# Kernel tuning notes

Hardware: AMD Instinct MI355X
Metric: run time of the kernel (lower is better)

Reference implementation:

```python
import jax, jax.numpy as jnp
import numpy as np

B, L = 128, 4096
H, RH, D, K = 128, 64, 64, 512  # num_hiddens, residual_hiddens, embedding_dim, num_embeddings
BETA = 0.25  # commitment_cost


def conv1d(x, w, b=None, stride=1, pad=0):
    # x: (N, C, W); w: (O, I, K) torch layout
    y = jax.lax.conv_general_dilated(x, w, (stride,), [(pad, pad)],
                                     dimension_numbers=('NCW', 'OIW', 'NCW'))
    return y if b is None else y + b[None, :, None]


def convT1d(x, w, b=None, stride=2, pad=1):
    # torch ConvTranspose1d weight layout (in, out, k)
    k = w.shape[-1]
    w_t = jnp.flip(w, -1).transpose(1, 0, 2)  # (out, in, k)
    y = jax.lax.conv_general_dilated(x, w_t, (1,), [(k - 1 - pad, k - 1 - pad)],
                                     lhs_dilation=(stride,),
                                     dimension_numbers=('NCW', 'OIW', 'NCW'))
    return y if b is None else y + b[None, :, None]


def res_stack(x, layers):
    for w1, w2 in layers:
        h = conv1d(jax.nn.relu(x), w1, None, 1, 1)
        h = conv1d(jax.nn.relu(h), w2, None, 1, 0)
        x = x + h
    return jax.nn.relu(x)


def _forward(x, enc_w1, enc_b1, enc_w2, enc_b2, enc_w3, enc_b3,
             enc_r1a, enc_r1b, enc_r2a, enc_r2b, pre_vq_w, pre_vq_b, codebook,
             dec_w1, dec_b1, dec_r1a, dec_r1b, dec_r2a, dec_r2b,
             dec_ct1_w, dec_ct1_b, dec_ct2_w, dec_ct2_b):
    # ---- Encoder (compression_factor == 4) ----
    h = x[:, None, :]                                   # (B, 1, L)
    h = jax.nn.relu(conv1d(h, enc_w1, enc_b1, 2, 1))    # (B, H/2, L/2)
    h = jax.nn.relu(conv1d(h, enc_w2, enc_b2, 2, 1))    # (B, H, L/4)
    h = conv1d(h, enc_w3, enc_b3, 1, 1)
    h = res_stack(h, [(enc_r1a, enc_r1b), (enc_r2a, enc_r2b)])
    z = conv1d(h, pre_vq_w, pre_vq_b, 1, 0)             # (B, D, T)

    # ---- Vector quantization ----
    zt = z.transpose(0, 2, 1)                           # (B, T, D)
    flat = zt.reshape(-1, D)                            # (BT, D)
    dists = (jnp.sum(flat * flat, 1, keepdims=True)
             - 2.0 * flat @ codebook.T
             + jnp.sum(codebook * codebook, 1))         # (BT, K)
    idx = jnp.argmin(dists, axis=1)                     # (BT,)
    q = codebook[idx].reshape(zt.shape)                 # (B, T, D)

    e_latent = jnp.mean((jax.lax.stop_gradient(q) - zt) ** 2)
    q_latent = jnp.mean((q - jax.lax.stop_gradient(zt)) ** 2)
    loss = q_latent + BETA * e_latent
    q_st = zt + jax.lax.stop_gradient(q - zt)           # straight-through

    counts = jnp.zeros((K,), flat.dtype).at[idx].add(1.0)
    probs = counts / idx.shape[0]
    perplexity = jnp.exp(-jnp.sum(probs * jnp.log(probs + 1e-10)))

    # ---- Decoder (compression_factor == 4) ----
    hd = q_st.transpose(0, 2, 1)                        # (B, D, T)
    hd = conv1d(hd, dec_w1, dec_b1, 1, 1)               # (B, H, T)
    hd = res_stack(hd, [(dec_r1a, dec_r1b), (dec_r2a, dec_r2b)])
    hd = jax.nn.relu(convT1d(hd, dec_ct1_w, dec_ct1_b)) # (B, H/2, 2T)
    hd = convT1d(hd, dec_ct2_w, dec_ct2_b)              # (B, 1, 4T)
    recon = jnp.squeeze(hd)                             # (B, L)
    return loss, recon, perplexity


def setup_inputs() -> dict:
    key = jax.random.key(0)
    ks = jax.random.split(key, 32)
    n = lambda i, shape, s=0.05: jax.random.normal(ks[i], shape, jnp.float32) * s
    inp = {
        'x': jax.random.normal(ks[0], (B, L), jnp.float32),
        'enc_w1': n(1, (H // 2, 1, 4)), 'enc_b1': jnp.zeros((H // 2,), jnp.float32),
        'enc_w2': n(2, (H, H // 2, 4)), 'enc_b2': jnp.zeros((H,), jnp.float32),
        'enc_w3': n(3, (H, H, 3)), 'enc_b3': jnp.zeros((H,), jnp.float32),
        'enc_r1a': n(4, (RH, H, 3)), 'enc_r1b': n(5, (H, RH, 1)),
        'enc_r2a': n(6, (RH, H, 3)), 'enc_r2b': n(7, (H, RH, 1)),
        'pre_vq_w': n(8, (D, H, 1)), 'pre_vq_b': jnp.zeros((D,), jnp.float32),
        'codebook': jax.random.uniform(ks[9], (K, D), jnp.float32, -1.0 / K, 1.0 / K),
        'dec_w1': n(10, (H, D, 3)), 'dec_b1': jnp.zeros((H,), jnp.float32),
        'dec_r1a': n(11, (RH, H, 3)), 'dec_r1b': n(12, (H, RH, 1)),
        'dec_r2a': n(13, (RH, H, 3)), 'dec_r2b': n(14, (H, RH, 1)),
        'dec_ct1_w': n(15, (H, H // 2, 4)), 'dec_ct1_b': jnp.zeros((H // 2,), jnp.float32),
        'dec_ct2_w': n(16, (H // 2, 1, 4)), 'dec_ct2_b': jnp.zeros((1,), jnp.float32),
    }
    return inp


def reference(x, enc_w1, enc_b1, enc_w2, enc_b2, enc_w3, enc_b3,
              enc_r1a, enc_r1b, enc_r2a, enc_r2b, pre_vq_w, pre_vq_b, codebook,
              dec_w1, dec_b1, dec_r1a, dec_r1b, dec_r2a, dec_r2b,
              dec_ct1_w, dec_ct1_b, dec_ct2_w, dec_ct2_b):
    return _forward(x, enc_w1, enc_b1, enc_w2, enc_b2, enc_w3, enc_b3,
                    enc_r1a, enc_r1b, enc_r2a, enc_r2b, pre_vq_w, pre_vq_b, codebook,
                    dec_w1, dec_b1, dec_r1a, dec_r1b, dec_r2a, dec_r2b,
                    dec_ct1_w, dec_ct1_b, dec_ct2_w, dec_ct2_b)
```

## Files before the change

kernel.cpp:

```cpp
#include <hip/hip_runtime.h>
#include <hip/hip_bf16.h>
#include <math.h>

using bf16 = __hip_bfloat16;
typedef __attribute__((ext_vector_type(4))) float f32x4;
typedef __attribute__((ext_vector_type(8))) short s16x8;

#define MFMA16(a,b,c) __builtin_amdgcn_mfma_f32_16x16x32_bf16((a),(b),(c),0,0,0)


__device__ inline float bf2f(unsigned short u) {
    union { float f; unsigned v; } c; c.v = ((unsigned)u) << 16; return c.f;
}
__device__ inline unsigned short bfbits(float f) {
    union { bf16 h; unsigned short u; } c; c.h = __float2bfloat16(f); return c.u;
}
__device__ inline s16x8 relu8(s16x8 v) {
#pragma unroll
    for (int j = 0; j < 8; ++j)
        v[j] = (short)(((unsigned short)v[j] & 0x8000u) ? 0 : (unsigned short)v[j]);
    return v;
}

__global__ __launch_bounds__(256, 3) void encmid_k(
    const bf16* __restrict__ in, const bf16* __restrict__ w3t,
    const float* __restrict__ b3, const bf16* __restrict__ r1w1,
    const bf16* __restrict__ r1w2, const bf16* __restrict__ r2w1,
    const bf16* __restrict__ r2w2, bf16* __restrict__ out)
{
    __shared__ __align__(16) char smem[47872];
    char* sY = smem;
    char* sX = smem + 21760;
    char* sH = smem + 21760;
    const int tid = threadIdx.x;
    const int b   = blockIdx.y;
    const int l0  = blockIdx.x * 64;
    const bf16* inb = in + (size_t)b * 1024 * 128;

    for (int i = tid; i < 96 * 16; i += 256) {
        int t = i >> 4, c0 = (i & 15) * 8;
        int g = l0 - 16 + t;
        s16x8 v = {};
        if (g >= 0 && g < 1024) v = *(const s16x8*)(inb + (size_t)g * 128 + c0);
        *(s16x8*)(sX + ((t * 136 + c0) << 1)) = v;
    }
    __syncthreads();

    const int lane = tid & 63;
    const int wid  = __builtin_amdgcn_readfirstlane(tid >> 6);
    const int lr   = lane & 15;
    const int kg   = lane >> 4;
    const f32x4 zf4 = {0.f, 0.f, 0.f, 0.f};

    {
        const int co0 = wid * 32;
        f32x4 acc[2][5];
#pragma unroll
        for (int cf = 0; cf < 2; ++cf)
#pragma unroll
            for (int lf = 0; lf < 5; ++lf) acc[cf][lf] = zf4;
#pragma unroll
        for (int k = 0; k < 3; ++k) {
            const bf16* Ab = w3t + (size_t)k * 128 * 128;
#pragma unroll
            for (int ks = 0; ks < 4; ++ks) {
                s16x8 af[2];
#pragma unroll
                for (int cf = 0; cf < 2; ++cf)
                    af[cf] = *(const s16x8*)(Ab + (co0 + cf * 16 + lr) * 128 + ks * 32 + kg * 8);
                s16x8 bfr[5];
#pragma unroll
                for (int lf = 0; lf < 5; ++lf) {
                    int tx = lf * 16 + lr + 7 + k;
                    bfr[lf] = *(const s16x8*)(sX + ((tx * 136 + ks * 32 + kg * 8) << 1));
                }
#pragma unroll
                for (int cf = 0; cf < 2; ++cf)
#pragma unroll
                    for (int lf = 0; lf < 5; ++lf)
                        acc[cf][lf] = MFMA16(af[cf], bfr[lf], acc[cf][lf]);
            }
        }
        __syncthreads();
#pragma unroll
        for (int cf = 0; cf < 2; ++cf)
#pragma unroll
            for (int lf = 0; lf < 5; ++lf) {
                int row = lf * 16 + lr;
                int p   = l0 - 8 + row;
                int cb0 = co0 + cf * 16 + kg * 4;
                bool ok = (p >= 0 && p < 1024);
                float r[4];
#pragma unroll
                for (int j = 0; j < 4; ++j)
                    r[j] = ok ? (acc[cf][lf][j] + b3[cb0 + j]) : 0.f;
                uint2 pk;
                pk.x = (unsigned)bfbits(r[0]) | ((unsigned)bfbits(r[1]) << 16);
                pk.y = (unsigned)bfbits(r[2]) | ((unsigned)bfbits(r[3]) << 16);
                *(uint2*)(sY + ((row * 136 + cb0) << 1)) = pk;
            }
    }
    __syncthreads();

#pragma unroll 1
    for (int blk = 0; blk < 2; ++blk) {
        const bf16* w1 = blk ? r2w1 : r1w1;
        {
            const int co0 = wid * 16;
            f32x4 acc[5];
#pragma unroll
            for (int lf = 0; lf < 5; ++lf) acc[lf] = zf4;
#pragma unroll
            for (int k = 0; k < 3; ++k) {
                const bf16* Ab = w1 + (size_t)k * 64 * 128;
#pragma unroll
                for (int ks = 0; ks < 4; ++ks) {
                    s16x8 a = *(const s16x8*)(Ab + (co0 + lr) * 128 + ks * 32 + kg * 8);
                    s16x8 bfr[5];
#pragma unroll
                    for (int lf = 0; lf < 5; ++lf) {
                        int ry = lf * 16 + lr + k - 1;
                        ry = (ry < 0) ? 0 : (ry > 79 ? 79 : ry);
                        bfr[lf] = relu8(*(const s16x8*)(sY + ((ry * 136 + ks * 32 + kg * 8) << 1)));
                    }
#pragma unroll
                    for (int lf = 0; lf < 5; ++lf)
                        acc[lf] = MFMA16(a, bfr[lf], acc[lf]);
                }
            }
#pragma unroll
            for (int lf = 0; lf < 5; ++lf) {
                int row = lf * 16 + lr;
                int ch0 = co0 + kg * 4;
                uint2 pk;
                pk.x = (unsigned)bfbits(fmaxf(acc[lf][0], 0.f)) |
                       ((unsigned)bfbits(fmaxf(acc[lf][1], 0.f)) << 16);
                pk.y = (unsigned)bfbits(fmaxf(acc[lf][2], 0.f)) |
                       ((unsigned)bfbits(fmaxf(acc[lf][3], 0.f)) << 16);
                *(uint2*)(sH + ((row * 72 + ch0) << 1)) = pk;
            }
        }
        __syncthreads();

        if (blk == 0) {
            const int co0 = wid * 32;
            f32x4 acc[2][5];
#pragma unroll
            for (int cf = 0; cf < 2; ++cf)
#pragma unroll
                for (int lf = 0; lf < 5; ++lf) acc[cf][lf] = zf4;
#pragma unroll
            for (int ks = 0; ks < 2; ++ks) {
                s16x8 af[2];
#pragma unroll
                for (int cf = 0; cf < 2; ++cf)
                    af[cf] = *(const s16x8*)(r1w2 + (size_t)(co0 + cf * 16 + lr) * 64 + ks * 32 + kg * 8);
                s16x8 bfr[5];
#pragma unroll
                for (int lf = 0; lf < 5; ++lf) {
                    int row = lf * 16 + lr;
                    bfr[lf] = *(const s16x8*)(sH + ((row * 72 + ks * 32 + kg * 8) << 1));
                }
#pragma unroll
                for (int cf = 0; cf < 2; ++cf)
#pragma unroll
                    for (int lf = 0; lf < 5; ++lf)
                        acc[cf][lf] = MFMA16(af[cf], bfr[lf], acc[cf][lf]);
            }
#pragma unroll
            for (int cf = 0; cf < 2; ++cf)
#pragma unroll
                for (int lf = 0; lf < 5; ++lf) {
                    int row = lf * 16 + lr;
                    int p   = l0 - 8 + row;
                    int cb0 = co0 + cf * 16 + kg * 4;
                    uint2 old = *(const uint2*)(sY + ((row * 136 + cb0) << 1));
                    bool ok = (p >= 0 && p < 1024);
                    float r[4];
                    r[0] = acc[cf][lf][0] + bf2f((unsigned short)(old.x & 0xffff));
                    r[1] = acc[cf][lf][1] + bf2f((unsigned short)(old.x >> 16));
                    r[2] = acc[cf][lf][2] + bf2f((unsigned short)(old.y & 0xffff));
                    r[3] = acc[cf][lf][3] + bf2f((unsigned short)(old.y >> 16));
                    uint2 pk;
                    pk.x = ok ? ((unsigned)bfbits(r[0]) | ((unsigned)bfbits(r[1]) << 16)) : 0u;
                    pk.y = ok ? ((unsigned)bfbits(r[2]) | ((unsigned)bfbits(r[3]) << 16)) : 0u;
                    *(uint2*)(sY + ((row * 136 + cb0) << 1)) = pk;
                }
            __syncthreads();
        } else {
            const int co0 = wid * 32;
            f32x4 acc[2][4];
#pragma unroll
            for (int cf = 0; cf < 2; ++cf)
#pragma unroll
                for (int lf = 0; lf < 4; ++lf) acc[cf][lf] = zf4;
#pragma unroll
            for (int ks = 0; ks < 2; ++ks) {
                s16x8 af[2];
#pragma unroll
                for (int cf = 0; cf < 2; ++cf)
                    af[cf] = *(const s16x8*)(r2w2 + (size_t)(co0 + cf * 16 + lr) * 64 + ks * 32 + kg * 8);
                s16x8 bfr[4];
#pragma unroll
                for (int lf = 0; lf < 4; ++lf) {
                    int row = 8 + lf * 16 + lr;
                    bfr[lf] = *(const s16x8*)(sH + ((row * 72 + ks * 32 + kg * 8) << 1));
                }
#pragma unroll
                for (int cf = 0; cf < 2; ++cf)
#pragma unroll
                    for (int lf = 0; lf < 4; ++lf)
                        acc[cf][lf] = MFMA16(af[cf], bfr[lf], acc[cf][lf]);
            }
#pragma unroll
            for (int cf = 0; cf < 2; ++cf)
#pragma unroll
                for (int lf = 0; lf < 4; ++lf) {
                    int row = 8 + lf * 16 + lr;
                    int cb0 = co0 + cf * 16 + kg * 4;
                    uint2 old = *(const uint2*)(sY + ((row * 136 + cb0) << 1));
                    float r[4];
                    r[0] = fmaxf(acc[cf][lf][0] + bf2f((unsigned short)(old.x & 0xffff)), 0.f);
                    r[1] = fmaxf(acc[cf][lf][1] + bf2f((unsigned short)(old.x >> 16)), 0.f);
                    r[2] = fmaxf(acc[cf][lf][2] + bf2f((unsigned short)(old.y & 0xffff)), 0.f);
                    r[3] = fmaxf(acc[cf][lf][3] + bf2f((unsigned short)(old.y >> 16)), 0.f);
                    uint2 pk;
                    pk.x = (unsigned)bfbits(r[0]) | ((unsigned)bfbits(r[1]) << 16);
                    pk.y = (unsigned)bfbits(r[2]) | ((unsigned)bfbits(r[3]) << 16);
                    *(uint2*)(out + ((size_t)b * 1024 + l0 + lf * 16 + lr) * 128 + cb0) = pk;
                }
        }
    }
}

__global__ __launch_bounds__(256, 4) void decmid_k(
    const bf16* __restrict__ qin, const bf16* __restrict__ dw1,
    const float* __restrict__ db1, const bf16* __restrict__ r1w1,
    const bf16* __restrict__ r1w2, const bf16* __restrict__ r2w1,
    const bf16* __restrict__ r2w2, const bf16* __restrict__ ct1w,
    const float* __restrict__ ct1b, bf16* __restrict__ out)
{
    __shared__ __align__(16) char smem[35584];
    char* sY = smem;
    char* sQ = smem + 21760;
    char* sH = smem + 21760;
    const int tid = threadIdx.x;
    const int b   = blockIdx.y;
    const int l0  = blockIdx.x * 64;
    const bf16* inb = qin + (size_t)b * 1024 * 64;

    for (int i = tid; i < 96 * 8; i += 256) {
        int t = i >> 3, c0 = (i & 7) * 8;
        int g = l0 - 16 + t;
        s16x8 v = {};
        if (g >= 0 && g < 1024) v = *(const s16x8*)(inb + (size_t)g * 64 + c0);
        *(s16x8*)(sQ + ((t * 72 + c0) << 1)) = v;
    }
    __syncthreads();

    const int lane = tid & 63;
    const int wid  = __builtin_amdgcn_readfirstlane(tid >> 6);
    const int lr   = lane & 15;
    const int kg   = lane >> 4;
    const f32x4 zf4 = {0.f, 0.f, 0.f, 0.f};

    {
        const int co0 = wid * 32;
        f32x4 acc[2][5];
#pragma unroll
        for (int cf = 0; cf < 2; ++cf)
#pragma unroll
            for (int lf = 0; lf < 5; ++lf) acc[cf][lf] = zf4;
#pragma unroll
        for (int k = 0; k < 3; ++k) {
            const bf16* Ab = dw1 + (size_t)k * 128 * 64;
#pragma unroll
            for (int ks = 0; ks < 2; ++ks) {
                s16x8 af[2];
#pragma unroll
                for (int cf = 0; cf < 2; ++cf)
                    af[cf] = *(const s16x8*)(Ab + (co0 + cf * 16 + lr) * 64 + ks * 32 + kg * 8);
                s16x8 bfr[5];
#pragma unroll
                for (int lf = 0; lf < 5; ++lf) {
                    int tx = lf * 16 + lr + 7 + k;
                    bfr[lf] = *(const s16x8*)(sQ + ((tx * 72 + ks * 32 + kg * 8) << 1));
                }
#pragma unroll
                for (int cf = 0; cf < 2; ++cf)
#pragma unroll
                    for (int lf = 0; lf < 5; ++lf)
                        acc[cf][lf] = MFMA16(af[cf], bfr[lf], acc[cf][lf]);
            }
        }
        __syncthreads();
#pragma unroll
        for (int cf = 0; cf < 2; ++cf)
#pragma unroll
            for (int lf = 0; lf < 5; ++lf) {
                int row = lf * 16 + lr;
                int p   = l0 - 8 + row;
                int cb0 = co0 + cf * 16 + kg * 4;
                bool ok = (p >= 0 && p < 1024);
                float r[4];
#pragma unroll
                for (int j = 0; j < 4; ++j)
                    r[j] = ok ? (acc[cf][lf][j] + db1[cb0 + j]) : 0.f;
                uint2 pk;
                pk.x = (unsigned)bfbits(r[0]) | ((unsigned)bfbits(r[1]) << 16);
                pk.y = (unsigned)bfbits(r[2]) | ((unsigned)bfbits(r[3]) << 16);
                *(uint2*)(sY + ((row * 136 + cb0) << 1)) = pk;
            }
    }
    __syncthreads();

#pragma unroll 1
    for (int blk = 0; blk < 2; ++blk) {
        const bf16* w1 = blk ? r2w1 : r1w1;
        const bf16* w2 = blk ? r2w2 : r1w2;
        {
            const int co0 = wid * 16;
            f32x4 acc[5];
#pragma unroll
            for (int lf = 0; lf < 5; ++lf) acc[lf] = zf4;
#pragma unroll
            for (int k = 0; k < 3; ++k) {
                const bf16* Ab = w1 + (size_t)k * 64 * 128;
#pragma unroll
                for (int ks = 0; ks < 4; ++ks) {
                    s16x8 a = *(const s16x8*)(Ab + (co0 + lr) * 128 + ks * 32 + kg * 8);
                    s16x8 bfr[5];
#pragma unroll
                    for (int lf = 0; lf < 5; ++lf) {
                        int ry = lf * 16 + lr + k - 1;
                        ry = (ry < 0) ? 0 : (ry > 79 ? 79 : ry);
                        bfr[lf] = relu8(*(const s16x8*)(sY + ((ry * 136 + ks * 32 + kg * 8) << 1)));
                    }
#pragma unroll
                    for (int lf = 0; lf < 5; ++lf)
                        acc[lf] = MFMA16(a, bfr[lf], acc[lf]);
                }
            }
#pragma unroll
            for (int lf = 0; lf < 5; ++lf) {
                int row = lf * 16 + lr;
                int ch0 = co0 + kg * 4;
                uint2 pk;
                pk.x = (unsigned)bfbits(fmaxf(acc[lf][0], 0.f)) |
                       ((unsigned)bfbits(fmaxf(acc[lf][1], 0.f)) << 16);
                pk.y = (unsigned)bfbits(fmaxf(acc[lf][2], 0.f)) |
                       ((unsigned)bfbits(fmaxf(acc[lf][3], 0.f)) << 16);
                *(uint2*)(sH + ((row * 72 + ch0) << 1)) = pk;
            }
        }
        __syncthreads();
        {
            const int co0 = wid * 32;
            f32x4 acc[2][5];
#pragma unroll
            for (int cf = 0; cf < 2; ++cf)
#pragma unroll
                for (int lf = 0; lf < 5; ++lf) acc[cf][lf] = zf4;
#pragma unroll
            for (int ks = 0; ks < 2; ++ks) {
                s16x8 af[2];
#pragma unroll
                for (int cf = 0; cf < 2; ++cf)
                    af[cf] = *(const s16x8*)(w2 + (size_t)(co0 + cf * 16 + lr) * 64 + ks * 32 + kg * 8);
                s16x8 bfr[5];
#pragma unroll
                for (int lf = 0; lf < 5; ++lf) {
                    int row = lf * 16 + lr;
                    bfr[lf] = *(const s16x8*)(sH + ((row * 72 + ks * 32 + kg * 8) << 1));
                }
#pragma unroll
                for (int cf = 0; cf < 2; ++cf)
#pragma unroll
                    for (int lf = 0; lf < 5; ++lf)
                        acc[cf][lf] = MFMA16(af[cf], bfr[lf], acc[cf][lf]);
            }
#pragma unroll
            for (int cf = 0; cf < 2; ++cf)
#pragma unroll
                for (int lf = 0; lf < 5; ++lf) {
                    int row = lf * 16 + lr;
                    int p   = l0 - 8 + row;
                    int cb0 = co0 + cf * 16 + kg * 4;
                    uint2 old = *(const uint2*)(sY + ((row * 136 + cb0) << 1));
                    bool ok = (p >= 0 && p < 1024);
                    float r[4];
                    r[0] = acc[cf][lf][0] + bf2f((unsigned short)(old.x & 0xffff));
                    r[1] = acc[cf][lf][1] + bf2f((unsigned short)(old.x >> 16));
                    r[2] = acc[cf][lf][2] + bf2f((unsigned short)(old.y & 0xffff));
                    r[3] = acc[cf][lf][3] + bf2f((unsigned short)(old.y >> 16));
                    if (blk == 1)
#pragma unroll
                        for (int j = 0; j < 4; ++j) r[j] = fmaxf(r[j], 0.f);
                    uint2 pk;
                    pk.x = ok ? ((unsigned)bfbits(r[0]) | ((unsigned)bfbits(r[1]) << 16)) : 0u;
                    pk.y = ok ? ((unsigned)bfbits(r[2]) | ((unsigned)bfbits(r[3]) << 16)) : 0u;
                    *(uint2*)(sY + ((row * 136 + cb0) << 1)) = pk;
                }
        }
        __syncthreads();
    }

    {
        const int co0 = (wid & 1) * 32;
        const int mh  = wid >> 1;
        f32x4 acc[2][2][2];
#pragma unroll
        for (int g = 0; g < 2; ++g)
#pragma unroll
            for (int cf = 0; cf < 2; ++cf)
#pragma unroll
                for (int j = 0; j < 2; ++j) acc[g][cf][j] = zf4;
#pragma unroll
        for (int g = 0; g < 2; ++g)
#pragma unroll
            for (int k = 0; k < 2; ++k) {
                const bf16* Ab = ct1w + (size_t)(g * 2 + k) * 64 * 128;
                const int doff = (g == 0) ? (k - 1) : k;
#pragma unroll
                for (int ks = 0; ks < 4; ++ks) {
                    s16x8 af[2];
#pragma unroll
                    for (int cf = 0; cf < 2; ++cf)
                        af[cf] = *(const s16x8*)(Ab + (co0 + cf * 16 + lr) * 128 + ks * 32 + kg * 8);
                    s16x8 bfr[2];
#pragma unroll
                    for (int j = 0; j < 2; ++j) {
                        int ty = 8 + (mh * 2 + j) * 16 + lr + doff;
                        bfr[j] = *(const s16x8*)(sY + ((ty * 136 + ks * 32 + kg * 8) << 1));
                    }
#pragma unroll
                    for (int cf = 0; cf < 2; ++cf)
#pragma unroll
                        for (int j = 0; j < 2; ++j)
                            acc[g][cf][j] = MFMA16(af[cf], bfr[j], acc[g][cf][j]);
                }
            }
#pragma unroll
        for (int g = 0; g < 2; ++g)
#pragma unroll
            for (int cf = 0; cf < 2; ++cf)
#pragma unroll
                for (int j = 0; j < 2; ++j) {
                    int m   = (mh * 2 + j) * 16 + lr;
                    int cb0 = co0 + cf * 16 + kg * 4;
                    float r[4];
#pragma unroll
                    for (int jj = 0; jj < 4; ++jj)
                        r[jj] = fmaxf(acc[g][cf][j][jj] + ct1b[cb0 + jj], 0.f);
                    uint2 pk;
                    pk.x = (unsigned)bfbits(r[0]) | ((unsigned)bfbits(r[1]) << 16);
                    pk.y = (unsigned)bfbits(r[2]) | ((unsigned)bfbits(r[3]) << 16);
                    *(uint2*)(out + ((size_t)b * 2048 + 2 * (l0 + m) + g) * 64 + cb0) = pk;
                }
    }
}

__global__ __launch_bounds__(256) void enc12_k(
    const float* __restrict__ x, const float* __restrict__ w1,
    const float* __restrict__ b1, const bf16* __restrict__ w2t,
    const float* __restrict__ b2, bf16* __restrict__ out)
{
    __shared__ float sXf[268];
    __shared__ float sW1[256];
    __shared__ float sB1[64];
    __shared__ __align__(16) char sX[132 * 144];
    const int tid = threadIdx.x;
    const int b   = blockIdx.y;
    const int l0  = blockIdx.x * 64;
    const float* xb = x + (size_t)b * 4096;

    for (int i = tid; i < 266; i += 256) {
        int g = 4 * l0 - 3 + i;
        sXf[i] = (g >= 0 && g < 4096) ? xb[g] : 0.f;
    }
    if (tid < 256) sW1[tid] = w1[tid];
    if (tid < 64)  sB1[tid] = b1[tid];
    __syncthreads();

    for (int i = tid; i < 132 * 64; i += 256) {
        int t = i >> 6, c = i & 63;
        int p = (t < 66) ? 2 * (l0 + t) : 2 * (l0 + t - 66) - 1;
        float v = 0.f;
        if (p >= 0 && p < 2048) {
            int xi = 2 * p - 4 * l0 + 2;
            float a = sB1[c];
#pragma unroll
            for (int k = 0; k < 4; ++k) a = fmaf(sXf[xi + k], sW1[c * 4 + k], a);
            v = fmaxf(a, 0.f);
        }
        *(bf16*)(sX + ((t * 72 + c) << 1)) = __float2bfloat16(v);
    }
    __syncthreads();

    const int lane = tid & 63;
    const int wid  = __builtin_amdgcn_readfirstlane(tid >> 6);
    const int co0  = wid * 32;
    const int lr   = lane & 15;
    const int kg   = lane >> 4;

    f32x4 acc[2][4];
#pragma unroll
    for (int cf = 0; cf < 2; ++cf)
#pragma unroll
        for (int lf = 0; lf < 4; ++lf) acc[cf][lf] = (f32x4){0.f, 0.f, 0.f, 0.f};

#pragma unroll
    for (int k = 0; k < 4; ++k) {
        const int roff = (k == 0) ? 66 : (k == 1) ? 0 : (k == 2) ? 67 : 1;
        const bf16* Ab = w2t + (size_t)k * 128 * 64;
#pragma unroll
        for (int ks = 0; ks < 2; ++ks) {
            s16x8 af[2];
#pragma unroll
            for (int cf = 0; cf < 2; ++cf)
                af[cf] = *(const s16x8*)(Ab + (co0 + cf * 16 + lr) * 64 + ks * 32 + kg * 8);
            s16x8 bfr[4];
#pragma unroll
            for (int lf = 0; lf < 4; ++lf) {
                int t = roff + lf * 16 + lr;
                bfr[lf] = *(const s16x8*)(sX + ((t * 72 + ks * 32 + kg * 8) << 1));
            }
#pragma unroll
            for (int cf = 0; cf < 2; ++cf)
#pragma unroll
                for (int lf = 0; lf < 4; ++lf)
                    acc[cf][lf] = MFMA16(af[cf], bfr[lf], acc[cf][lf]);
        }
    }

#pragma unroll
    for (int cf = 0; cf < 2; ++cf)
#pragma unroll
        for (int lf = 0; lf < 4; ++lf) {
            int cb0  = co0 + cf * 16 + kg * 4;
            int lcol = lf * 16 + lr;
            float r[4];
#pragma unroll
            for (int j = 0; j < 4; ++j)
                r[j] = fmaxf(acc[cf][lf][j] + b2[cb0 + j], 0.f);
            uint2 pk;
            pk.x = (unsigned)bfbits(r[0]) | ((unsigned)bfbits(r[1]) << 16);
            pk.y = (unsigned)bfbits(r[2]) | ((unsigned)bfbits(r[3]) << 16);
            *(uint2*)(out + ((size_t)b * 1024 + l0 + lcol) * 128 + cb0) = pk;
        }
}

__global__ __launch_bounds__(256) void ct2_k(
    const bf16* __restrict__ in, const float* __restrict__ w,
    const float* __restrict__ bias, float* __restrict__ out)
{
    __shared__ __align__(16) char sX[258 * 144];
    const int tid = threadIdx.x;
    const int b   = blockIdx.y;
    const int m0  = blockIdx.x * 256;
    const bf16* inb = in + (size_t)b * 2048 * 64;
    for (int i = tid; i < 258 * 8; i += 256) {
        int t = i >> 3, c0 = (i & 7) * 8;
        int g = m0 - 1 + t;
        s16x8 v = {};
        if (g >= 0 && g < 2048) v = *(const s16x8*)(inb + (size_t)g * 64 + c0);
        *(s16x8*)(sX + ((t * 72 + c0) << 1)) = v;
    }
    __syncthreads();
    float e = bias[0], o = bias[0];
#pragma unroll
    for (int c0 = 0; c0 < 64; c0 += 8) {
        s16x8 vm1 = *(const s16x8*)(sX + (((tid + 0) * 72 + c0) << 1));
        s16x8 v0  = *(const s16x8*)(sX + (((tid + 1) * 72 + c0) << 1));
        s16x8 vp1 = *(const s16x8*)(sX + (((tid + 2) * 72 + c0) << 1));
#pragma unroll
        for (int j = 0; j < 8; ++j) {
            int ci = c0 + j;
            float xm1 = bf2f((unsigned short)vm1[j]);
            float x0  = bf2f((unsigned short)v0[j]);
            float xp1 = bf2f((unsigned short)vp1[j]);
            e = fmaf(x0,  w[ci * 4 + 1], fmaf(xm1, w[ci * 4 + 3], e));
            o = fmaf(xp1, w[ci * 4 + 0], fmaf(x0,  w[ci * 4 + 2], o));
        }
    }
    int m = m0 + tid;
    out[(size_t)b * 4096 + 2 * m]     = e;
    out[(size_t)b * 4096 + 2 * m + 1] = o;
}

__global__ __launch_bounds__(256) void wx_k(
    const float* ew2, const float* ew3, const float* er1a, const float* er1b,
    const float* er2a, const float* er2b, const float* pvw, const float* dw1,
    const float* dr1a, const float* dr1b, const float* dr2a, const float* dr2b,
    const float* ct1w, bf16* wb)
{
    const int job = blockIdx.x;
    bf16* dst = wb + (size_t)job * 65536;
    const float* src; int CO, CI, K;
    switch (job) {
        case 0:  src = ew2;  CO = 128; CI = 64;  K = 4; break;
        case 1:  src = ew3;  CO = 128; CI = 128; K = 3; break;
        case 2:  src = er1a; CO = 64;  CI = 128; K = 3; break;
        case 3:  src = er1b; CO = 128; CI = 64;  K = 1; break;
        case 4:  src = er2a; CO = 64;  CI = 128; K = 3; break;
        case 5:  src = er2b; CO = 128; CI = 64;  K = 1; break;
        case 6:  src = pvw;  CO = 64;  CI = 128; K = 1; break;
        case 7:  src = dw1;  CO = 128; CI = 64;  K = 3; break;
        case 8:  src = dr1a; CO = 64;  CI = 128; K = 3; break;
        case 9:  src = dr1b; CO = 128; CI = 64;  K = 1; break;
        case 10: src = dr2a; CO = 64;  CI = 128; K = 3; break;
        case 11: src = dr2b; CO = 128; CI = 64;  K = 1; break;
        default: src = ct1w; CO = 64;  CI = 128; K = 4; break;
    }
    const int tot = CO * CI * K;
    for (int i = blockIdx.y * 256 + threadIdx.x; i < tot; i += gridDim.y * 256) {
        if (job < 12) {
            int k = i / (CO * CI); int r = i - k * CO * CI;
            int co = r / CI; int ci = r - co * CI;
            dst[i] = __float2bfloat16(src[((size_t)co * CI + ci) * K + k]);
        } else {
            const int TAP[4] = {3, 1, 2, 0};
            int g = i / (64 * 128); int r = i - g * 64 * 128;
            int co = r / 128; int ci = r - co * 128;
            dst[i] = __float2bfloat16(src[((size_t)ci * 64 + co) * 4 + TAP[g]]);
        }
    }
}

__global__ __launch_bounds__(256) void cbprep_k(
    const float* __restrict__ cb, bf16* __restrict__ cbh, bf16* __restrict__ cbl,
    float* __restrict__ sc)
{
    int k = blockIdx.x * 256 + threadIdx.x;
    const float* c = cb + (size_t)k * 64;
    float s = 0.f;
#pragma unroll
    for (int d = 0; d < 64; ++d) s = fmaf(c[d], c[d], s);
    sc[k] = s;
#pragma unroll
    for (int c0 = 0; c0 < 64; c0 += 8) {
        union { unsigned short u[8]; s16x8 v; } ph, pl;
#pragma unroll
        for (int j = 0; j < 8; ++j) {
            float v = c[c0 + j];
            unsigned short h = bfbits(v);
            ph.u[j] = h;
            pl.u[j] = bfbits(v - bf2f(h));
        }
        *(s16x8*)(cbh + (size_t)k * 64 + c0) = ph.v;
        *(s16x8*)(cbl + (size_t)k * 64 + c0) = pl.v;
    }
}

__global__ __launch_bounds__(256, 4) void vqf_k(
    const bf16* __restrict__ A, const bf16* __restrict__ pvw,
    const float* __restrict__ pvb, const float* __restrict__ cbf,
    const bf16* __restrict__ cbh, const bf16* __restrict__ cbl,
    const float* __restrict__ sc, bf16* __restrict__ q,
    float* __restrict__ counts, float* __restrict__ loss_sum)
{
    __shared__ __align__(16) char sMem[34816];
    __shared__ float sSC[512];
    __shared__ float sHist[512];
    __shared__ int   sBK[128];
    __shared__ float sWS[4];
    const int tid = threadIdx.x;
    sSC[tid] = sc[tid]; sSC[tid + 256] = sc[tid + 256];
    sHist[tid] = 0.f;   sHist[tid + 256] = 0.f;

    const int n0 = blockIdx.x * 128;
    for (int i = tid; i < 128 * 16; i += 256) {
        int t = i >> 4, c0 = (i & 15) * 8;
        s16x8 v = *(const s16x8*)(A + (size_t)(n0 + t) * 128 + c0);
        *(s16x8*)(sMem + ((t * 136 + c0) << 1)) = v;
    }
    __syncthreads();

    const int lane = tid & 63, wid = tid >> 6;
    const int lr = lane & 15, kg = lane >> 4;
    const int pw0 = wid * 32;
    const f32x4 zf4 = {0.f, 0.f, 0.f, 0.f};

    f32x4 zacc[4][2];
#pragma unroll
    for (int cf = 0; cf < 4; ++cf)
#pragma unroll
        for (int lf = 0; lf < 2; ++lf) zacc[cf][lf] = zf4;
#pragma unroll
    for (int ks = 0; ks < 4; ++ks) {
        s16x8 af[4];
#pragma unroll
        for (int cf = 0; cf < 4; ++cf)
            af[cf] = *(const s16x8*)(pvw + (size_t)(cf * 16 + lr) * 128 + ks * 32 + kg * 8);
        s16x8 bfr[2];
#pragma unroll
        for (int lf = 0; lf < 2; ++lf) {
            int t = pw0 + lf * 16 + lr;
            bfr[lf] = *(const s16x8*)(sMem + ((t * 136 + ks * 32 + kg * 8) << 1));
        }
#pragma unroll
        for (int cf = 0; cf < 4; ++cf)
#pragma unroll
            for (int lf = 0; lf < 2; ++lf)
                zacc[cf][lf] = MFMA16(af[cf], bfr[lf], zacc[cf][lf]);
    }
    __syncthreads();

#pragma unroll
    for (int cf = 0; cf < 4; ++cf)
#pragma unroll
        for (int lf = 0; lf < 2; ++lf) {
            int pos = pw0 + lf * 16 + lr;
            int ch  = cf * 16 + kg * 4;
            float4 v = make_float4(zacc[cf][lf][0] + pvb[ch],
                                   zacc[cf][lf][1] + pvb[ch + 1],
                                   zacc[cf][lf][2] + pvb[ch + 2],
                                   zacc[cf][lf][3] + pvb[ch + 3]);
            *(float4*)(sMem + (pos * 68 + ch) * 4) = v;
        }
    __syncthreads();

    s16x8 bh[2][2], bl[2][2];
#pragma unroll
    for (int lf = 0; lf < 2; ++lf)
#pragma unroll
        for (int ks = 0; ks < 2; ++ks) {
            int t = pw0 + lf * 16 + lr;
            int ch = ks * 32 + kg * 8;
            float4 v0 = *(const float4*)(sMem + (t * 68 + ch) * 4);
            float4 v1 = *(const float4*)(sMem + (t * 68 + ch) * 4 + 16);
            float v[8] = {v0.x, v0.y, v0.z, v0.w, v1.x, v1.y, v1.z, v1.w};
            union { unsigned short u[8]; s16x8 s; } ph, pl;
#pragma unroll
            for (int j = 0; j < 8; ++j) {
                unsigned short h = bfbits(v[j]);
                ph.u[j] = h;
                pl.u[j] = bfbits(v[j] - bf2f(h));
            }
            bh[lf][ks] = ph.s; bl[lf][ks] = pl.s;
        }

    float bestd[2] = {3.4e38f, 3.4e38f};
    int   bestk[2] = {0, 0};
#pragma unroll 2
    for (int cf = 0; cf < 32; ++cf) {
        int code = cf * 16 + lr;
        const bf16* ph = cbh + code * 64 + kg * 8;
        const bf16* pl = cbl + code * 64 + kg * 8;
        s16x8 ah0 = *(const s16x8*)ph;
        s16x8 ah1 = *(const s16x8*)(ph + 32);
        s16x8 al0 = *(const s16x8*)pl;
        s16x8 al1 = *(const s16x8*)(pl + 32);
        float s0 = sSC[cf * 16 + kg * 4 + 0];
        float s1 = sSC[cf * 16 + kg * 4 + 1];
        float s2 = sSC[cf * 16 + kg * 4 + 2];
        float s3 = sSC[cf * 16 + kg * 4 + 3];
        int kb = cf * 16 + kg * 4;
#pragma unroll
        for (int lf = 0; lf < 2; ++lf) {
            f32x4 acc = MFMA16(ah0, bh[lf][0], zf4);
            acc = MFMA16(ah1, bh[lf][1], acc);
            acc = MFMA16(al0, bh[lf][0], acc);
            acc = MFMA16(al1, bh[lf][1], acc);
            acc = MFMA16(ah0, bl[lf][0], acc);
            acc = MFMA16(ah1, bl[lf][1], acc);
            float d0 = fmaf(acc[0], -2.f, s0);
            float d1 = fmaf(acc[1], -2.f, s1);
            float d2 = fmaf(acc[2], -2.f, s2);
            float d3 = fmaf(acc[3], -2.f, s3);
            if (d0 < bestd[lf]) { bestd[lf] = d0; bestk[lf] = kb; }
            if (d1 < bestd[lf]) { bestd[lf] = d1; bestk[lf] = kb + 1; }
            if (d2 < bestd[lf]) { bestd[lf] = d2; bestk[lf] = kb + 2; }
            if (d3 < bestd[lf]) { bestd[lf] = d3; bestk[lf] = kb + 3; }
        }
    }
#pragma unroll
    for (int lf = 0; lf < 2; ++lf) {
#pragma unroll
        for (int off = 16; off <= 32; off <<= 1) {
            float od = __shfl_xor(bestd[lf], off, 64);
            int   ok = __shfl_xor(bestk[lf], off, 64);
            if (od < bestd[lf] || (od == bestd[lf] && ok < bestk[lf])) {
                bestd[lf] = od; bestk[lf] = ok;
            }
        }
        if (kg == 0) sBK[pw0 + lf * 16 + lr] = bestk[lf];
    }
    __syncthreads();

    const int pos  = tid >> 1;
    const int half = tid & 1;
    const int k = sBK[pos];
    if (half == 0) atomicAdd(&sHist[k], 1.f);
    float lsum = 0.f;
    const float* qp = cbf + (size_t)k * 64 + half * 32;
    bf16* qo = q + (size_t)(n0 + pos) * 64 + half * 32;
#pragma unroll
    for (int c0 = 0; c0 < 32; c0 += 8) {
        int zb = (pos * 68 + half * 32 + c0) * 4;
        float4 z0 = *(const float4*)(sMem + zb);
        float4 z1 = *(const float4*)(sMem + zb + 16);
        float4 q0 = *(const float4*)(qp + c0);
        float4 q1 = *(const float4*)(qp + c0 + 4);
        float qv[8] = {q0.x, q0.y, q0.z, q0.w, q1.x, q1.y, q1.z, q1.w};
        float zv[8] = {z0.x, z0.y, z0.z, z0.w, z1.x, z1.y, z1.z, z1.w};
        union { unsigned short u[8]; s16x8 v; } pk;
#pragma unroll
        for (int j = 0; j < 8; ++j) {
            float d = qv[j] - zv[j];
            lsum = fmaf(d, d, lsum);
            pk.u[j] = bfbits(qv[j]);
        }
        *(s16x8*)(qo + c0) = pk.v;
    }
#pragma unroll
    for (int off = 32; off > 0; off >>= 1) lsum += __shfl_down(lsum, off, 64);
    if ((tid & 63) == 0) sWS[tid >> 6] = lsum;
    __syncthreads();
    if (tid == 0) atomicAdd(loss_sum, sWS[0] + sWS[1] + sWS[2] + sWS[3]);
    float c0v = sHist[tid];       if (c0v != 0.f) atomicAdd(&counts[tid], c0v);
    float c1v = sHist[tid + 256]; if (c1v != 0.f) atomicAdd(&counts[tid + 256], c1v);
}

__global__ __launch_bounds__(512) void finalize_k(
    const float* __restrict__ counts, const float* __restrict__ loss_sum,
    float* __restrict__ d_out, int out_size)
{
    __shared__ float ws2[8];
    const int tid = threadIdx.x;
    float p = counts[tid] * (1.f / 131072.f);
    float e = p * logf(p + 1e-10f);
#pragma unroll
    for (int off = 32; off > 0; off >>= 1) e += __shfl_down(e, off, 64);
    const int lane = tid & 63, wid = tid >> 6;
    if (lane == 0) ws2[wid] = e;
    __syncthreads();
    if (tid == 0) {
        float s = 0.f;
        for (int i = 0; i < 8; ++i) s += ws2[i];
        d_out[0] = 1.25f * loss_sum[0] * (1.f / 8388608.f);
        d_out[out_size - 1] = expf(-s);
    }
}

extern "C" void kernel_launch(void* const* d_in, const int* in_sizes, int n_in,
                              void* d_out, int out_size, void* d_ws, size_t ws_size,
                              hipStream_t stream)
{
    const float* x        = (const float*)d_in[0];
    const float* enc_w1   = (const float*)d_in[1];
    const float* enc_b1   = (const float*)d_in[2];
    const float* enc_b2   = (const float*)d_in[4];
    const float* enc_b3   = (const float*)d_in[6];
    const float* pre_vq_b = (const float*)d_in[12];
    const float* cb       = (const float*)d_in[13];
    const float* dec_b1   = (const float*)d_in[15];
    const float* ct1_b    = (const float*)d_in[21];
    const float* ct2_w    = (const float*)d_in[22];
    const float* ct2_b    = (const float*)d_in[23];
    float* out = (float*)d_out;

    char* base = (char*)d_ws;
    bf16*  wb   = (bf16*)base;
    bf16*  Abf  = (bf16*)(base + ((size_t)2   << 20));
    bf16*  Bbf  = (bf16*)(base + ((size_t)40  << 20));
    bf16*  Qbf  = (bf16*)(base + ((size_t)78  << 20));
    bf16*  cbh  = (bf16*)(base + ((size_t)96  << 20));
    bf16*  cbl  = (bf16*)(base + ((size_t)96  << 20) + 65536);
    float* sc   = (float*)(base + ((size_t)96  << 20) + 131072);
    float* cnt  = sc + 512;
    float* lsum = cnt + 512;

    (void)hipMemsetAsync(cnt, 0, 513 * sizeof(float), stream);

    dim3 blk(256);
    dim3 g16(16, 128);

    wx_k<<<dim3(13, 8), blk, 0, stream>>>(
        (const float*)d_in[3], (const float*)d_in[5], (const float*)d_in[7],
        (const float*)d_in[8], (const float*)d_in[9], (const float*)d_in[10],
        (const float*)d_in[11], (const float*)d_in[14], (const float*)d_in[16],
        (const float*)d_in[17], (const float*)d_in[18], (const float*)d_in[19],
        (const float*)d_in[20], wb);
    cbprep_k<<<2, blk, 0, stream>>>(cb, cbh, cbl, sc);

    enc12_k<<<g16, blk, 0, stream>>>(x, enc_w1, enc_b1, wb + 0 * 65536, enc_b2, Bbf);
    encmid_k<<<g16, blk, 0, stream>>>(Bbf, wb + 1 * 65536, enc_b3,
        wb + 2 * 65536, wb + 3 * 65536, wb + 4 * 65536, wb + 5 * 65536, Abf);

    vqf_k<<<1024, blk, 0, stream>>>(Abf, wb + 6 * 65536, pre_vq_b, cb,
                                    cbh, cbl, sc, Qbf, cnt, lsum);

    decmid_k<<<g16, blk, 0, stream>>>(Qbf, wb + 7 * 65536, dec_b1,
        wb + 8 * 65536, wb + 9 * 65536, wb + 10 * 65536, wb + 11 * 65536,
        wb + 12 * 65536, ct1_b, Bbf);

    ct2_k<<<dim3(8, 128), blk, 0, stream>>>(Bbf, ct2_w, ct2_b, out + 1);
    finalize_k<<<1, 512, 0, stream>>>(cnt, lsum, out, out_size);
}
```

Before: 357.6 us.

## Shrink conv halo in fused encoder/decoder mid kernels and stage ct1 output via LDS

Reduces the halo rows loaded and kept in shared memory for the fused encoder and decoder residual-stack kernels from 16 down to the 2-4 actually needed, clamping tile reads and skipping stores for rows past the valid range. The smaller LDS footprint allows raising launch_bounds occupancy (3→4 and 4→5 blocks). The decoder's transposed-conv output is also staged through shared memory and written with contiguous 16-byte stores instead of scattered 8-byte writes. MFMA fragment counts stay the same, so the redundant compute is not removed, only the memory and LDS pressure.

Measured after the change: 444.5 us. 24.3% more time.

```diff
diff --git a/kernel.cpp b/kernel.cpp
--- a/kernel.cpp
+++ b/kernel.cpp
@@ -21,25 +21,31 @@
         v[j] = (short)(((unsigned short)v[j] & 0x8000u) ? 0 : (unsigned short)v[j]);
     return v;
 }
-
-__global__ __launch_bounds__(256, 3) void encmid_k(
+__device__ inline uint2 pack4(float a, float b, float c, float d) {
+    uint2 p;
+    p.x = (unsigned)bfbits(a) | ((unsigned)bfbits(b) << 16);
+    p.y = (unsigned)bfbits(c) | ((unsigned)bfbits(d) << 16);
+    return p;
+}
+
+__global__ __launch_bounds__(256, 4) void encmid_k(
     const bf16* __restrict__ in, const bf16* __restrict__ w3t,
     const float* __restrict__ b3, const bf16* __restrict__ r1w1,
     const bf16* __restrict__ r1w2, const bf16* __restrict__ r2w1,
     const bf16* __restrict__ r2w2, bf16* __restrict__ out)
 {
-    __shared__ __align__(16) char smem[47872];
+    __shared__ __align__(16) char smem[37536];
     char* sY = smem;
-    char* sX = smem + 21760;
-    char* sH = smem + 21760;
+    char* sX = smem + 18496;
+    char* sH = smem + 18496;
     const int tid = threadIdx.x;
     const int b   = blockIdx.y;
     const int l0  = blockIdx.x * 64;
     const bf16* inb = in + (size_t)b * 1024 * 128;
 
-    for (int i = tid; i < 96 * 16; i += 256) {
+    for (int i = tid; i < 70 * 16; i += 256) {
         int t = i >> 4, c0 = (i & 15) * 8;
-        int g = l0 - 16 + t;
+        int g = l0 - 3 + t;
         s16x8 v = {};
         if (g >= 0 && g < 1024) v = *(const s16x8*)(inb + (size_t)g * 128 + c0);
         *(s16x8*)(sX + ((t * 136 + c0) << 1)) = v;
@@ -71,7 +77,8 @@
                 s16x8 bfr[5];
 #pragma unroll
                 for (int lf = 0; lf < 5; ++lf) {
-                    int tx = lf * 16 + lr + 7 + k;
+                    int tx = lf * 16 + lr + k;
+                    tx = (tx > 69) ? 69 : tx;
                     bfr[lf] = *(const s16x8*)(sX + ((tx * 136 + ks * 32 + kg * 8) << 1));
                 }
 #pragma unroll
@@ -87,24 +94,24 @@
 #pragma unroll
             for (int lf = 0; lf < 5; ++lf) {
                 int row = lf * 16 + lr;
-                int p   = l0 - 8 + row;
-                int cb0 = co0 + cf * 16 + kg * 4;
-                bool ok = (p >= 0 && p < 1024);
-                float r[4];
-#pragma unroll
-                for (int j = 0; j < 4; ++j)
-                    r[j] = ok ? (acc[cf][lf][j] + b3[cb0 + j]) : 0.f;
-                uint2 pk;
-                pk.x = (unsigned)bfbits(r[0]) | ((unsigned)bfbits(r[1]) << 16);
-                pk.y = (unsigned)bfbits(r[2]) | ((unsigned)bfbits(r[3]) << 16);
-                *(uint2*)(sY + ((row * 136 + cb0) << 1)) = pk;
+                if (row < 68) {
+                    int p   = l0 - 2 + row;
+                    int cb0 = co0 + cf * 16 + kg * 4;
+                    bool ok = (p >= 0 && p < 1024);
+                    float r[4];
+#pragma unroll
+                    for (int j = 0; j < 4; ++j)
+                        r[j] = ok ? (acc[cf][lf][j] + b3[cb0 + j]) : 0.f;
+                    *(uint2*)(sY + ((row * 136 + cb0) << 1)) = pack4(r[0], r[1], r[2], r[3]);
+                }
             }
     }
     __syncthreads();
 
 #pragma unroll 1
-    for (int blk = 0; blk < 2; ++blk) {
-        const bf16* w1 = blk ? r2w1 : r1w1;
+    for (int blk2 = 0; blk2 < 2; ++blk2) {
+        const bf16* w1 = blk2 ? r2w1 : r1w1;
+        const bf16* w2 = blk2 ? r2w2 : r1w2;
         {
             const int co0 = wid * 16;
             f32x4 acc[5];
@@ -120,7 +127,7 @@
 #pragma unroll
                     for (int lf = 0; lf < 5; ++lf) {
                         int ry = lf * 16 + lr + k - 1;
-                        ry = (ry < 0) ? 0 : (ry > 79 ? 79 : ry);
+                        ry = (ry < 0) ? 0 : (ry > 67 ? 67 : ry);
                         bfr[lf] = relu8(*(const s16x8*)(sY + ((ry * 136 + ks * 32 + kg * 8) << 1)));
                     }
 #pragma unroll
@@ -131,18 +138,17 @@
 #pragma unroll
             for (int lf = 0; lf < 5; ++lf) {
                 int row = lf * 16 + lr;
-                int ch0 = co0 + kg * 4;
-                uint2 pk;
-                pk.x = (unsigned)bfbits(fmaxf(acc[lf][0], 0.f)) |
-                       ((unsigned)bfbits(fmaxf(acc[lf][1], 0.f)) << 16);
-                pk.y = (unsigned)bfbits(fmaxf(acc[lf][2], 0.f)) |
-                       ((unsigned)bfbits(fmaxf(acc[lf][3], 0.f)) << 16);
-                *(uint2*)(sH + ((row * 72 + ch0) << 1)) = pk;
+                if (row < 68) {
+                    int ch0 = co0 + kg * 4;
+                    *(uint2*)(sH + ((row * 72 + ch0) << 1)) =
+                        pack4(fmaxf(acc[lf][0], 0.f), fmaxf(acc[lf][1], 0.f),
+                              fmaxf(acc[lf][2], 0.f), fmaxf(acc[lf][3], 0.f));
+                }
             }
         }
         __syncthreads();
 
-        if (blk == 0) {
+        if (blk2 == 0) {
             const int co0 = wid * 32;
             f32x4 acc[2][5];
 #pragma unroll
@@ -159,7 +165,8 @@
 #pragma unroll
                 for (int lf = 0; lf < 5; ++lf) {
                     int row = lf * 16 + lr;
-                    bfr[lf] = *(const s16x8*)(sH + ((row * 72 + ks * 32 + kg * 8) << 1));
+                    int rc  = (row > 67) ? 67 : row;
+                    bfr[lf] = *(const s16x8*)(sH + ((rc * 72 + ks * 32 + kg * 8) << 1));
                 }
 #pragma unroll
                 for (int cf = 0; cf < 2; ++cf)
@@ -172,19 +179,19 @@
 #pragma unroll
                 for (int lf = 0; lf < 5; ++lf) {
                     int row = lf * 16 + lr;
-                    int p   = l0 - 8 + row;
-                    int cb0 = co0 + cf * 16 + kg * 4;
-                    uint2 old = *(const uint2*)(sY + ((row * 136 + cb0) << 1));
-                    bool ok = (p >= 0 && p < 1024);
-                    float r[4];
-                    r[0] = acc[cf][lf][0] + bf2f((unsigned short)(old.x & 0xffff));
-                    r[1] = acc[cf][lf][1] + bf2f((unsigned short)(old.x >> 16));
-                    r[2] = acc[cf][lf][2] + bf2f((unsigned short)(old.y & 0xffff));
-                    r[3] = acc[cf][lf][3] + bf2f((unsigned short)(old.y >> 16));
-                    uint2 pk;
-                    pk.x = ok ? ((unsigned)bfbits(r[0]) | ((unsigned)bfbits(r[1]) << 16)) : 0u;
-                    pk.y = ok ? ((unsigned)bfbits(r[2]) | ((unsigned)bfbits(r[3]) << 16)) : 0u;
-                    *(uint2*)(sY + ((row * 136 + cb0) << 1)) = pk;
+                    if (row < 68) {
+                        int p   = l0 - 2 + row;
+                        int cb0 = co0 + cf * 16 + kg * 4;
+                        uint2 old = *(const uint2*)(sY + ((row * 136 + cb0) << 1));
+                        bool ok = (p >= 0 && p < 1024);
+                        float r0 = acc[cf][lf][0] + bf2f((unsigned short)(old.x & 0xffff));
+                        float r1 = acc[cf][lf][1] + bf2f((unsigned short)(old.x >> 16));
+                        float r2 = acc[cf][lf][2] + bf2f((unsigned short)(old.y & 0xffff));
+                        float r3 = acc[cf][lf][3] + bf2f((unsigned short)(old.y >> 16));
+                        uint2 pk = pack4(r0, r1, r2, r3);
+                        if (!ok) { pk.x = 0u; pk.y = 0u; }
+                        *(uint2*)(sY + ((row * 136 + cb0) << 1)) = pk;
+                    }
                 }
             __syncthreads();
         } else {
@@ -203,7 +210,7 @@
                 s16x8 bfr[4];
 #pragma unroll
                 for (int lf = 0; lf < 4; ++lf) {
-                    int row = 8 + lf * 16 + lr;
+                    int row = 2 + lf * 16 + lr;
                     bfr[lf] = *(const s16x8*)(sH + ((row * 72 + ks * 32 + kg * 8) << 1));
                 }
 #pragma unroll
@@ -216,42 +223,39 @@
             for (int cf = 0; cf < 2; ++cf)
 #pragma unroll
                 for (int lf = 0; lf < 4; ++lf) {
-                    int row = 8 + lf * 16 + lr;
+                    int row = 2 + lf * 16 + lr;
                     int cb0 = co0 + cf * 16 + kg * 4;
                     uint2 old = *(const uint2*)(sY + ((row * 136 + cb0) << 1));
-                    float r[4];
-                    r[0] = fmaxf(acc[cf][lf][0] + bf2f((unsigned short)(old.x & 0xffff)), 0.f);
-                    r[1] = fmaxf(acc[cf][lf][1] + bf2f((unsigned short)(old.x >> 16)), 0.f);
-                    r[2] = fmaxf(acc[cf][lf][2] + bf2f((unsigned short)(old.y & 0xffff)), 0.f);
-                    r[3] = fmaxf(acc[cf][lf][3] + bf2f((unsigned short)(old.y >> 16)), 0.f);
-                    uint2 pk;
-                    pk.x = (unsigned)bfbits(r[0]) | ((unsigned)bfbits(r[1]) << 16);
-                    pk.y = (unsigned)bfbits(r[2]) | ((unsigned)bfbits(r[3]) << 16);
-                    *(uint2*)(out + ((size_t)b * 1024 + l0 + lf * 16 + lr) * 128 + cb0) = pk;
-                }
-        }
-    }
-}
-
-__global__ __launch_bounds__(256, 4) void decmid_k(
+                    float r0 = fmaxf(acc[cf][lf][0] + bf2f((unsigned short)(old.x & 0xffff)), 0.f);
+                    float r1 = fmaxf(acc[cf][lf][1] + bf2f((unsigned short)(old.x >> 16)), 0.f);
+                    float r2 = fmaxf(acc[cf][lf][2] + bf2f((unsigned short)(old.y & 0xffff)), 0.f);
+                    float r3 = fmaxf(acc[cf][lf][3] + bf2f((unsigned short)(old.y >> 16)), 0.f);
+                    *(uint2*)(out + ((size_t)b * 1024 + l0 + lf * 16 + lr) * 128 + cb0) =
+                        pack4(r0, r1, r2, r3);
+                }
+        }
+    }
+}
+
+__global__ __launch_bounds__(256, 5) void decmid_k(
     const bf16* __restrict__ qin, const bf16* __restrict__ dw1,
     const float* __restrict__ db1, const bf16* __restrict__ r1w1,
     const bf16* __restrict__ r1w2, const bf16* __restrict__ r2w1,
     const bf16* __restrict__ r2w2, const bf16* __restrict__ ct1w,
     const float* __restrict__ ct1b, bf16* __restrict__ out)
 {
-    __shared__ __align__(16) char smem[35584];
+    __shared__ __align__(16) char smem[29408];
     char* sY = smem;
-    char* sQ = smem + 21760;
-    char* sH = smem + 21760;
+    char* sQ = smem + 19040;
+    char* sH = smem + 19040;
     const int tid = threadIdx.x;
     const int b   = blockIdx.y;
     const int l0  = blockIdx.x * 64;
     const bf16* inb = qin + (size_t)b * 1024 * 64;
 
-    for (int i = tid; i < 96 * 8; i += 256) {
+    for (int i = tid; i < 72 * 8; i += 256) {
         int t = i >> 3, c0 = (i & 7) * 8;
-        int g = l0 - 16 + t;
+        int g = l0 - 4 + t;
         s16x8 v = {};
         if (g >= 0 && g < 1024) v = *(const s16x8*)(inb + (size_t)g * 64 + c0);
         *(s16x8*)(sQ + ((t * 72 + c0) << 1)) = v;
@@ -283,7 +287,8 @@
                 s16x8 bfr[5];
 #pragma unroll
                 for (int lf = 0; lf < 5; ++lf) {
-                    int tx = lf * 16 + lr + 7 + k;
+                    int tx = lf * 16 + lr + k;
+                    tx = (tx > 71) ? 71 : tx;
                     bfr[lf] = *(const s16x8*)(sQ + ((tx * 72 + ks * 32 + kg * 8) << 1));
                 }
 #pragma unroll
@@ -299,25 +304,24 @@
 #pragma unroll
             for (int lf = 0; lf < 5; ++lf) {
                 int row = lf * 16 + lr;
-                int p   = l0 - 8 + row;
-                int cb0 = co0 + cf * 16 + kg * 4;
-                bool ok = (p >= 0 && p < 1024);
-                float r[4];
-#pragma unroll
-                for (int j = 0; j < 4; ++j)
-                    r[j] = ok ? (acc[cf][lf][j] + db1[cb0 + j]) : 0.f;
-                uint2 pk;
-                pk.x = (unsigned)bfbits(r[0]) | ((unsigned)bfbits(r[1]) << 16);
-                pk.y = (unsigned)bfbits(r[2]) | ((unsigned)bfbits(r[3]) << 16);
-                *(uint2*)(sY + ((row * 136 + cb0) << 1)) = pk;
+                if (row < 70) {
+                    int p   = l0 - 3 + row;
+                    int cb0 = co0 + cf * 16 + kg * 4;
+                    bool ok = (p >= 0 && p < 1024);
+                    float r[4];
+#pragma unroll
+                    for (int j = 0; j < 4; ++j)
+                        r[j] = ok ? (acc[cf][lf][j] + db1[cb0 + j]) : 0.f;
+                    *(uint2*)(sY + ((row * 136 + cb0) << 1)) = pack4(r[0], r[1], r[2], r[3]);
+                }
             }
     }
     __syncthreads();
 
 #pragma unroll 1
-    for (int blk = 0; blk < 2; ++blk) {
-        const bf16* w1 = blk ? r2w1 : r1w1;
-        const bf16* w2 = blk ? r2w2 : r1w2;
+    for (int blk2 = 0; blk2 < 2; ++blk2) {
+        const bf16* w1 = blk2 ? r2w1 : r1w1;
+        const bf16* w2 = blk2 ? r2w2 : r1w2;
         {
             const int co0 = wid * 16;
             f32x4 acc[5];
@@ -333,7 +337,7 @@
 #pragma unroll
                     for (int lf = 0; lf < 5; ++lf) {
                         int ry = lf * 16 + lr + k - 1;
-                        ry = (ry < 0) ? 0 : (ry > 79 ? 79 : ry);
+                        ry = (ry < 0) ? 0 : (ry > 69 ? 69 : ry);
                         bfr[lf] = relu8(*(const s16x8*)(sY + ((ry * 136 + ks * 32 + kg * 8) << 1)));
                     }
 #pragma unroll
@@ -344,13 +348,12 @@
 #pragma unroll
             for (int lf = 0; lf < 5; ++lf) {
                 int row = lf * 16 + lr;
-                int ch0 = co0 + kg * 4;
-                uint2 pk;
-                pk.x = (unsigned)bfbits(fmaxf(acc[lf][0], 0.f)) |
-                       ((unsigned)bfbits(fmaxf(acc[lf][1], 0.f)) << 16);
-                pk.y = (unsigned)bfbits(fmaxf(acc[lf][2], 0.f)) |
-                       ((unsigned)bfbits(fmaxf(acc[lf][3], 0.f)) << 16);
-                *(uint2*)(sH + ((row * 72 + ch0) << 1)) = pk;
+                if (row < 70) {
+                    int ch0 = co0 + kg * 4;
+                    *(uint2*)(sH + ((row * 72 + ch0) << 1)) =
+                        pack4(fmaxf(acc[lf][0], 0.f), fmaxf(acc[lf][1], 0.f),
+                              fmaxf(acc[lf][2], 0.f), fmaxf(acc[lf][3], 0.f));
+                }
             }
         }
         __syncthreads();
@@ -371,7 +374,8 @@
 #pragma unroll
                 for (int lf = 0; lf < 5; ++lf) {
                     int row = lf * 16 + lr;
-                    bfr[lf] = *(const s16x8*)(sH + ((row * 72 + ks * 32 + kg * 8) << 1));
+                    int rc  = (row > 69) ? 69 : row;
+                    bfr[lf] = *(const s16x8*)(sH + ((rc * 72 + ks * 32 + kg * 8) << 1));
                 }
 #pragma unroll
                 for (int cf = 0; cf < 2; ++cf)
@@ -384,22 +388,23 @@
 #pragma unroll
                 for (int lf = 0; lf < 5; ++lf) {
                     int row = lf * 16 + lr;
-                    int p   = l0 - 8 + row;
-                    int cb0 = co0 + cf * 16 + kg * 4;
-                    uint2 old = *(const uint2*)(sY + ((row * 136 + cb0) << 1));
-                    bool ok = (p >= 0 && p < 1024);
-                    float r[4];
-                    r[0] = acc[cf][lf][0] + bf2f((unsigned short)(old.x & 0xffff));
-                    r[1] = acc[cf][lf][1] + bf2f((unsigned short)(old.x >> 16));
-                    r[2] = acc[cf][lf][2] + bf2f((unsigned short)(old.y & 0xffff));
-                    r[3] = acc[cf][lf][3] + bf2f((unsigned short)(old.y >> 16));
-                    if (blk == 1)
-#pragma unroll
-                        for (int j = 0; j < 4; ++j) r[j] = fmaxf(r[j], 0.f);
-                    uint2 pk;
-                    pk.x = ok ? ((unsigned)bfbits(r[0]) | ((unsigned)bfbits(r[1]) << 16)) : 0u;
-                    pk.y = ok ? ((unsigned)bfbits(r[2]) | ((unsigned)bfbits(r[3]) << 16)) : 0u;
-                    *(uint2*)(sY + ((row * 136 + cb0) << 1)) = pk;
+                    if (row < 70) {
+                        int p   = l0 - 3 + row;
+                        int cb0 = co0 + cf * 16 + kg * 4;
+                        uint2 old = *(const uint2*)(sY + ((row * 136 + cb0) << 1));
+                        bool ok = (p >= 0 && p < 1024);
+                        float r0 = acc[cf][lf][0] + bf2f((unsigned short)(old.x & 0xffff));
+                        float r1 = acc[cf][lf][1] + bf2f((unsigned short)(old.x >> 16));
+                        float r2 = acc[cf][lf][2] + bf2f((unsigned short)(old.y & 0xffff));
+                        float r3 = acc[cf][lf][3] + bf2f((unsigned short)(old.y >> 16));
+                        if (blk2 == 1) {
+                            r0 = fmaxf(r0, 0.f); r1 = fmaxf(r1, 0.f);
+                            r2 = fmaxf(r2, 0.f); r3 = fmaxf(r3, 0.f);
+                        }
+                        uint2 pk = pack4(r0, r1, r2, r3);
+                        if (!ok) { pk.x = 0u; pk.y = 0u; }
+                        *(uint2*)(sY + ((row * 136 + cb0) << 1)) = pk;
+                    }
                 }
         }
         __syncthreads();
@@ -430,7 +435,7 @@
                     s16x8 bfr[2];
 #pragma unroll
                     for (int j = 0; j < 2; ++j) {
-                        int ty = 8 + (mh * 2 + j) * 16 + lr + doff;
+                        int ty = 3 + (mh * 2 + j) * 16 + lr + doff;
                         bfr[j] = *(const s16x8*)(sY + ((ty * 136 + ks * 32 + kg * 8) << 1));
                     }
 #pragma unroll
@@ -440,6 +445,8 @@
                             acc[g][cf][j] = MFMA16(af[cf], bfr[j], acc[g][cf][j]);
                 }
             }
+        __syncthreads();
+
 #pragma unroll
         for (int g = 0; g < 2; ++g)
 #pragma unroll
@@ -447,16 +454,19 @@
 #pragma unroll
                 for (int j = 0; j < 2; ++j) {
                     int m   = (mh * 2 + j) * 16 + lr;
-                    int cb0 = co0 + cf * 16 + kg * 4;
+                    int rr  = 2 * m + g;
+                    int ch0 = co0 + cf * 16 + kg * 4;
                     float r[4];
 #pragma unroll
                     for (int jj = 0; jj < 4; ++jj)
-                        r[jj] = fmaxf(acc[g][cf][j][jj] + ct1b[cb0 + jj], 0.f);
-                    uint2 pk;
-                    pk.x = (unsigned)bfbits(r[0]) | ((unsigned)bfbits(r[1]) << 16);
-                    pk.y = (unsigned)bfbits(r[2]) | ((unsigned)bfbits(r[3]) << 16);
-                    *(uint2*)(out + ((size_t)b * 2048 + 2 * (l0 + m) + g) * 64 + cb0) = pk;
-                }
+                        r[jj] = fmaxf(acc[g][cf][j][jj] + ct1b[ch0 + jj], 0.f);
+                    *(uint2*)(sY + rr * 128 + ch0 * 2) = pack4(r[0], r[1], r[2], r[3]);
+                }
+        __syncthreads();
+
+        bf16* ob = out + ((size_t)b * 2048 + 2 * l0) * 64;
+        for (int i = tid; i < 1024; i += 256)
+            *(s16x8*)(ob + i * 8) = *(const s16x8*)(sY + i * 16);
     }
 }
 
@@ -543,10 +553,8 @@
 #pragma unroll
             for (int j = 0; j < 4; ++j)
                 r[j] = fmaxf(acc[cf][lf][j] + b2[cb0 + j], 0.f);
-            uint2 pk;
-            pk.x = (unsigned)bfbits(r[0]) | ((unsigned)bfbits(r[1]) << 16);
-            pk.y = (unsigned)bfbits(r[2]) | ((unsigned)bfbits(r[3]) << 16);
-            *(uint2*)(out + ((size_t)b * 1024 + l0 + lcol) * 128 + cb0) = pk;
+            *(uint2*)(out + ((size_t)b * 1024 + l0 + lcol) * 128 + cb0) =
+                pack4(r[0], r[1], r[2], r[3]);
         }
 }
 
```
